# Kernel optimization log

Hardware: AMD Instinct MI355X
Metric: run time of the kernel (lower is better)

Reference implementation:

```python
import jax, jax.numpy as jnp
import numpy as np

DIM, H, KV, S, B = 2048, 16, 4, 2048, 2
HD = DIM // H
REP = H // KV
EPS = 1e-6

def rotate_half(x):
    x1, x2 = x[..., :HD // 2], x[..., HD // 2:]
    return jnp.concatenate([-x2, x1], axis=-1)

def setup_inputs() -> dict:
    key = jax.random.key(0)
    ks = jax.random.split(key, 6)
    x = jax.random.normal(ks[0], (B, S, DIM), dtype=jnp.float32)
    sc = 1.0 / np.sqrt(DIM)
    Wq = jax.random.normal(ks[1], (DIM, H * HD), dtype=jnp.float32) * sc
    Wk = jax.random.normal(ks[2], (DIM, KV * HD), dtype=jnp.float32) * sc
    Wv = jax.random.normal(ks[3], (DIM, KV * HD), dtype=jnp.float32) * sc
    Wo = jax.random.normal(ks[4], (H * HD, DIM), dtype=jnp.float32) * sc
    qg = jnp.ones((HD,), dtype=jnp.float32)
    kg = jnp.ones((HD,), dtype=jnp.float32)
    # RoPE tables (cached buffers in the torch module)
    inv_freq = 1.0 / (10000.0 ** (jnp.arange(0, HD, 2, dtype=jnp.float32) / HD))
    freqs = jnp.arange(S, dtype=jnp.float32)[:, None] * inv_freq[None, :]
    emb = jnp.concatenate([freqs, freqs], axis=-1)  # [S, HD]
    cos, sin = jnp.cos(emb), jnp.sin(emb)
    # causal additive mask [1,1,S,S]
    mask = jnp.where(jnp.tril(jnp.ones((S, S), dtype=bool)), 0.0, -1e9)[None, None].astype(jnp.float32)
    return {"x": x, "Wq": Wq, "Wk": Wk, "Wv": Wv, "Wo": Wo,
            "qg": qg, "kg": kg, "cos": cos, "sin": sin, "mask": mask}

def rmsnorm(x, g):
    rms = jnp.sqrt(jnp.mean(x * x, axis=-1, keepdims=True) + EPS)
    return g * (x / rms)

def reference(x, Wq, Wk, Wv, Wo, qg, kg, cos, sin, mask):
    Bx, Sx, _ = x.shape
    q = (x @ Wq).reshape(Bx, Sx, H, HD).transpose(0, 2, 1, 3)   # [B,H,S,HD]
    k = (x @ Wk).reshape(Bx, Sx, KV, HD).transpose(0, 2, 1, 3)  # [B,KV,S,HD]
    v = (x @ Wv).reshape(Bx, Sx, KV, HD).transpose(0, 2, 1, 3)
    q = rmsnorm(q, qg)
    k = rmsnorm(k, kg)
    c = cos[None, None, :Sx, :]
    s = sin[None, None, :Sx, :]
    q = q * c + rotate_half(q) * s
    k = k * c + rotate_half(k) * s
    k = jnp.repeat(k, REP, axis=1)  # [B,H,S,HD]
    v = jnp.repeat(v, REP, axis=1)
    scale = 1.0 / np.sqrt(HD)
    scores = jnp.einsum('bhqd,bhkd->bhqk', q, k) * scale + mask
    attn = jax.nn.softmax(scores, axis=-1)
    out = jnp.einsum('bhqk,bhkd->bhqd', attn, v)
    out = out.transpose(0, 2, 1, 3).reshape(Bx, Sx, H * HD)
    return out @ Wo
```

## Files before the change

### kernel.cpp

```cpp
#include <hip/hip_runtime.h>

typedef unsigned short u16;
typedef __attribute__((ext_vector_type(8))) short s16x8;
typedef __attribute__((ext_vector_type(4))) float f32x4;
typedef __attribute__((ext_vector_type(4))) unsigned short u16x4;

#define DIMSZ 2048
#define NH    16
#define NKV   4
#define SEQ   2048
#define BB    2
#define HD    128
#define REPF  4
#define SCALE 0.08838834764831845f

__device__ __forceinline__ u16 f2bf(float x) {
  union { float f; unsigned u; } v; v.f = x;
  unsigned r = v.u + 0x7fffu + ((v.u >> 16) & 1u);
  return (u16)(r >> 16);
}
__device__ __forceinline__ float bf2f(u16 x) {
  union { unsigned u; float f; } v; v.u = ((unsigned)x) << 16;
  return v.f;
}
__device__ __forceinline__ unsigned pack2(float a, float b) {
  union { float f; unsigned u; } x, y; x.f = a; y.f = b;
  return ((x.u + 0x8000u) >> 16) | ((y.u + 0x8000u) & 0xffff0000u);
}
__device__ __forceinline__ void gld16(const void* g, void* l) {
  __builtin_amdgcn_global_load_lds(
      (const __attribute__((address_space(1))) unsigned int*)g,
      (__attribute__((address_space(3))) unsigned int*)l, 16, 0, 0);
}

#define BARX __builtin_amdgcn_s_barrier()
#define LG0  do { asm volatile("s_waitcnt lgkmcnt(0)" ::: "memory"); \
                  __builtin_amdgcn_sched_barrier(0); } while (0)
#define VMW(n) asm volatile("s_waitcnt vmcnt(" #n ")" ::: "memory")

__global__ __launch_bounds__(256) void k_cvt(const float* __restrict__ x,
                                             u16* __restrict__ o) {
  int i = (blockIdx.x * 256 + threadIdx.x) * 8;
  float4 a = *(const float4*)(x + i);
  float4 b = *(const float4*)(x + i + 4);
  u16x4 p0 = { f2bf(a.x), f2bf(a.y), f2bf(a.z), f2bf(a.w) };
  u16x4 p1 = { f2bf(b.x), f2bf(b.y), f2bf(b.z), f2bf(b.w) };
  *(u16x4*)(o + i) = p0;
  *(u16x4*)(o + i + 4) = p1;
}

__global__ __launch_bounds__(256) void k_transpose(const float* __restrict__ W,
                                                   u16* __restrict__ Wt,
                                                   int K, int N) {
  __shared__ float t[32][33];
  int tx = threadIdx.x & 31, ty = threadIdx.x >> 5;
  int r0 = blockIdx.y * 32, c0 = blockIdx.x * 32;
#pragma unroll
  for (int i = 0; i < 32; i += 8)
    t[ty + i][tx] = W[(size_t)(r0 + ty + i) * N + c0 + tx];
  __syncthreads();
#pragma unroll
  for (int i = 0; i < 32; i += 8)
    Wt[(size_t)(c0 + ty + i) * K + r0 + tx] = f2bf(t[tx][ty + i]);
}

__global__ __launch_bounds__(512, 2) void k_gemm256(const u16* __restrict__ A,
                                                    const u16* __restrict__ Bt,
                                                    void* __restrict__ C0,
                                                    void* __restrict__ C1,
                                                    void* __restrict__ C2,
                                                    int M, int N, int K, int mode) {
  __shared__ __align__(16) u16 shA[2][256 * 64];
  __shared__ __align__(16) u16 shB[2][256 * 64];
  const int tid = threadIdx.x;
  const int wave = tid >> 6, lane = tid & 63;
  const int l15 = lane & 15, lh = lane >> 4;
  const int wm = wave >> 2, wn = wave & 3;
  const int m0 = blockIdx.y * 256, n0 = blockIdx.x * 256;

  const int srow = wave * 8 + (lane >> 3);
  const int sgr = ((lane & 7) ^ ((lane >> 3) & 7)) * 8;
  const u16* gA = A + (size_t)(m0 + srow) * K + sgr;
  const u16* gB = Bt + (size_t)(n0 + srow) * K + sgr;

  auto stgA = [&](int rb, int kt, int sl) {
    gld16(gA + (size_t)rb * 64 * K + (size_t)kt * 64, &shA[sl][rb * 4096 + wave * 512]);
  };
  auto stgB = [&](int rb, int kt, int sl) {
    gld16(gB + (size_t)rb * 64 * K + (size_t)kt * 64, &shB[sl][rb * 4096 + wave * 512]);
  };
  auto rdA = [&](int mf, int ks, int sl) -> s16x8 {
    int rl = wm * 128 + mf * 16 + l15;
    return *(const s16x8*)&shA[sl][rl * 64 + (((ks * 4 + lh) ^ (l15 & 7)) * 8)];
  };
  auto rdB = [&](int nf, int ks, int sl) -> s16x8 {
    int rl = wn * 64 + nf * 16 + l15;
    return *(const s16x8*)&shB[sl][rl * 64 + (((ks * 4 + lh) ^ (l15 & 7)) * 8)];
  };

  f32x4 acc[8][4] = {};
  s16x8 afr[4], bfr[4];
  const int NK = K >> 6;

  stgB(0, 0, 0); stgB(1, 0, 0); stgB(2, 0, 0); stgB(3, 0, 0);
  stgA(0, 0, 0); stgA(2, 0, 0); stgA(1, 0, 0); stgA(3, 0, 0);
  VMW(2);
  BARX;

  for (int t = 0; t < NK; ++t) {
    const int sl = t & 1, ns = sl ^ 1;
    const bool st = (t + 1 < NK);
    const int kn = t + 1;

#pragma unroll
    for (int nf = 0; nf < 4; nf++) bfr[nf] = rdB(nf, 0, sl);
#pragma unroll
    for (int i = 0; i < 4; i++) afr[i] = rdA(i, 0, sl);
    if (st) { stgB(0, kn, ns); stgB(1, kn, ns); }
    BARX; LG0;
    __builtin_amdgcn_s_setprio(1);
#pragma unroll
    for (int i = 0; i < 4; i++)
#pragma unroll
      for (int nf = 0; nf < 4; nf++)
        acc[i][nf] = __builtin_amdgcn_mfma_f32_16x16x32_bf16(afr[i], bfr[nf], acc[i][nf], 0, 0, 0);
    __builtin_amdgcn_s_setprio(0);
    if (st) VMW(2); else VMW(0);
    BARX;

#pragma unroll
    for (int i = 0; i < 4; i++) afr[i] = rdA(4 + i, 0, sl);
    if (st) { stgB(2, kn, ns); stgB(3, kn, ns); }
    BARX; LG0;
    __builtin_amdgcn_s_setprio(1);
#pragma unroll
    for (int i = 0; i < 4; i++)
#pragma unroll
      for (int nf = 0; nf < 4; nf++)
        acc[4 + i][nf] = __builtin_amdgcn_mfma_f32_16x16x32_bf16(afr[i], bfr[nf], acc[4 + i][nf], 0, 0, 0);
    __builtin_amdgcn_s_setprio(0);
    BARX;

#pragma unroll
    for (int nf = 0; nf < 4; nf++) bfr[nf] = rdB(nf, 1, sl);
#pragma unroll
    for (int i = 0; i < 4; i++) afr[i] = rdA(i, 1, sl);
    if (st) { stgA(0, kn, ns); stgA(2, kn, ns); }
    BARX; LG0;
    __builtin_amdgcn_s_setprio(1);
#pragma unroll
    for (int i = 0; i < 4; i++)
#pragma unroll
      for (int nf = 0; nf < 4; nf++)
        acc[i][nf] = __builtin_amdgcn_mfma_f32_16x16x32_bf16(afr[i], bfr[nf], acc[i][nf], 0, 0, 0);
    __builtin_amdgcn_s_setprio(0);
    BARX;

#pragma unroll
    for (int i = 0; i < 4; i++) afr[i] = rdA(4 + i, 1, sl);
    if (st) { stgA(1, kn, ns); stgA(3, kn, ns); }
    BARX; LG0;
    __builtin_amdgcn_s_setprio(1);
#pragma unroll
    for (int i = 0; i < 4; i++)
#pragma unroll
      for (int nf = 0; nf < 4; nf++)
        acc[4 + i][nf] = __builtin_amdgcn_mfma_f32_16x16x32_bf16(afr[i], bfr[nf], acc[4 + i][nf], 0, 0, 0);
    __builtin_amdgcn_s_setprio(0);
    if (st) VMW(2);
    BARX;
  }

  if (mode == 1) {
    float* C = (float*)C0;
#pragma unroll
    for (int mf = 0; mf < 8; mf++)
#pragma unroll
      for (int nf = 0; nf < 4; nf++)
#pragma unroll
        for (int r = 0; r < 4; r++) {
          int m = m0 + wm * 128 + mf * 16 + lh * 4 + r;
          int n = n0 + wn * 64 + nf * 16 + l15;
          C[(size_t)m * N + n] = acc[mf][nf][r];
        }
  } else {
    if (n0 < 2048) {
      u16* C = (u16*)C0;
#pragma unroll
      for (int mf = 0; mf < 8; mf++)
#pragma unroll
        for (int nf = 0; nf < 4; nf++)
#pragma unroll
          for (int r = 0; r < 4; r++) {
            int m = m0 + wm * 128 + mf * 16 + lh * 4 + r;
            int n = n0 + wn * 64 + nf * 16 + l15;
            C[(size_t)m * 2048 + n] = f2bf(acc[mf][nf][r]);
          }
    } else if (n0 < 2560) {
      u16* C = (u16*)C1;
#pragma unroll
      for (int mf = 0; mf < 8; mf++)
#pragma unroll
        for (int nf = 0; nf < 4; nf++)
#pragma unroll
          for (int r = 0; r < 4; r++) {
            int m = m0 + wm * 128 + mf * 16 + lh * 4 + r;
            int n = n0 - 2048 + wn * 64 + nf * 16 + l15;
            C[(size_t)m * 512 + n] = f2bf(acc[mf][nf][r]);
          }
    } else {
      u16* C = (u16*)C2;
#pragma unroll
      for (int mf = 0; mf < 8; mf++)
#pragma unroll
        for (int nf = 0; nf < 4; nf++) {
          int n = n0 - 2560 + wn * 64 + nf * 16 + l15;
          int kvh = n >> 7, d = n & 127;
          int m = m0 + wm * 128 + mf * 16 + lh * 4;
          int b = m >> 11, s = m & 2047;
          u16x4 pk = { f2bf(acc[mf][nf][0]), f2bf(acc[mf][nf][1]),
                       f2bf(acc[mf][nf][2]), f2bf(acc[mf][nf][3]) };
          *(u16x4*)&C[(((size_t)b * NKV + kvh) * HD + d) * SEQ + s] = pk;
        }
    }
  }
}

__global__ __launch_bounds__(256) void k_normrope(u16* __restrict__ Q,
                                                  u16* __restrict__ Kb,
                                                  const float* __restrict__ qg,
                                                  const float* __restrict__ kg,
                                                  const float* __restrict__ cosT,
                                                  const float* __restrict__ sinT) {
  int wid = (blockIdx.x * 256 + threadIdx.x) >> 6;
  int lane = threadIdx.x & 63;
  const int NQR = BB * SEQ * NH;
  u16* ptr; const float* g; int s;
  if (wid < NQR) {
    ptr = Q + (size_t)wid * HD; g = qg; s = (wid / NH) % SEQ;
  } else {
    int r2 = wid - NQR;
    ptr = Kb + (size_t)r2 * HD; g = kg; s = (r2 / NKV) % SEQ;
  }
  int d = lane * 2;
  unsigned v = *(const unsigned*)(ptr + d);
  float x0 = bf2f((u16)(v & 0xffff)), x1 = bf2f((u16)(v >> 16));
  float ss = x0 * x0 + x1 * x1;
#pragma unroll
  for (int off = 32; off >= 1; off >>= 1) ss += __shfl_xor(ss, off);
  float rinv = rsqrtf(ss * (1.0f / HD) + 1e-6f);
  float2 gv = *(const float2*)&g[d];
  float n0 = x0 * rinv * gv.x, n1 = x1 * rinv * gv.y;
  float p0 = __shfl_xor(n0, 32), p1 = __shfl_xor(n1, 32);
  float r0 = (lane < 32) ? -p0 : p0;
  float r1 = (lane < 32) ? -p1 : p1;
  float2 cc = *(const float2*)&cosT[s * HD + d];
  float2 sn = *(const float2*)&sinT[s * HD + d];
  float o0 = n0 * cc.x + r0 * sn.x, o1 = n1 * cc.y + r1 * sn.y;
  *(unsigned*)(ptr + d) = (unsigned)f2bf(o0) | ((unsigned)f2bf(o1) << 16);
}

__global__ __launch_bounds__(512, 2) void k_attn(const u16* __restrict__ Q,
                                                 const u16* __restrict__ Kb,
                                                 const u16* __restrict__ Vt,
                                                 u16* __restrict__ O) {
  __shared__ __align__(16) u16 shK[2][64 * 128];
  __shared__ __align__(16) u16 shV[2][128 * 64];
  __shared__ __align__(16) u16 shP[8][16 * 72];
  const int tid = threadIdx.x, wave = tid >> 6, lane = tid & 63;
  const int l15 = lane & 15, lh = lane >> 4;
  const int bid = blockIdx.x;
  const int qt = 15 - (bid >> 5);
  const int bh = bid & 31, b = bh >> 4, h = bh & 15, kvh = h >> 2;
  const int q0w = qt * 128 + wave * 16;

  const u16* qbase = Q + ((size_t)((size_t)b * SEQ + q0w + l15) * NH + h) * HD;
  s16x8 qf[4];
#pragma unroll
  for (int kf = 0; kf < 4; kf++) qf[kf] = *(const s16x8*)(qbase + kf * 32 + lh * 8);

  const u16* srcK[2]; const u16* srcV[2];
  int dstK[2], dstV[2];
#pragma unroll
  for (int c = 0; c < 2; c++) {
    int rk = c * 32 + wave * 4 + (lane >> 4);
    int gk = (lane & 15) ^ (rk & 7);
    srcK[c] = Kb + ((size_t)((size_t)b * SEQ + rk) * NKV + kvh) * HD + gk * 8;
    dstK[c] = (c * 32 + wave * 4) * 128;
    int rv = c * 64 + wave * 8 + (lane >> 3);
    int gv = (lane & 7) ^ (rv & 7);
    srcV[c] = Vt + ((size_t)((size_t)b * NKV + kvh) * HD + rv) * SEQ + gv * 8;
    dstV[c] = (c * 64 + wave * 8) * 64;
  }

  f32x4 oacc[8] = {};
  float m = -3e38f, l = 0.f;
  const int nt = qt * 2 + 2;
  const int tmask = q0w >> 6;
  const float SC2 = SCALE * 1.44269504f;

#pragma unroll
  for (int c = 0; c < 2; c++) {
    gld16(srcK[c], &shK[0][dstK[c]]);
    gld16(srcV[c], &shV[0][dstV[c]]);
  }
  __syncthreads();

  int buf = 0;
  for (int kt = 0; kt < nt; kt++) {
    if (kt + 1 < nt) {
      const size_t koff = (size_t)(kt + 1) * 64;
#pragma unroll
      for (int c = 0; c < 2; c++) {
        gld16(srcK[c] + koff * (NKV * HD), &shK[buf ^ 1][dstK[c]]);
        gld16(srcV[c] + koff, &shV[buf ^ 1][dstV[c]]);
      }
    }

    f32x4 sacc[4] = {};
    __builtin_amdgcn_s_setprio(1);
#pragma unroll
    for (int kf = 0; kf < 4; kf++)
#pragma unroll
      for (int nf = 0; nf < 4; nf++) {
        s16x8 kfr = *(const s16x8*)&shK[buf][(nf * 16 + l15) * 128 + (((kf * 4 + lh) ^ (l15 & 7)) * 8)];
        sacc[nf] = __builtin_amdgcn_mfma_f32_16x16x32_bf16(kfr, qf[kf], sacc[nf], 0, 0, 0);
      }
    __builtin_amdgcn_s_setprio(0);

    const int q = q0w + l15;
    float p[4][4];
    float mx = -3e38f;
    if (kt >= tmask) {
#pragma unroll
      for (int nf = 0; nf < 4; nf++)
#pragma unroll
        for (int r = 0; r < 4; r++) {
          int k = kt * 64 + nf * 16 + lh * 4 + r;
          float s = (k <= q) ? sacc[nf][r] * SC2 : -3e38f;
          p[nf][r] = s; mx = fmaxf(mx, s);
        }
    } else {
#pragma unroll
      for (int nf = 0; nf < 4; nf++)
#pragma unroll
        for (int r = 0; r < 4; r++) {
          float s = sacc[nf][r] * SC2;
          p[nf][r] = s; mx = fmaxf(mx, s);
        }
    }
    mx = fmaxf(mx, __shfl_xor(mx, 16));
    mx = fmaxf(mx, __shfl_xor(mx, 32));

    if (!__all(mx - m <= 8.0f)) {
      float mnew = fmaxf(m, mx);
      float alpha = exp2f(m - mnew);
      l *= alpha; m = mnew;
#pragma unroll
      for (int r = 0; r < 4; r++) {
        float ar = __shfl(alpha, (lh << 2) | r);
#pragma unroll
        for (int nf = 0; nf < 8; nf++) oacc[nf][r] *= ar;
      }
    }

    float rs = 0.f;
#pragma unroll
    for (int nf = 0; nf < 4; nf++)
#pragma unroll
      for (int r = 0; r < 4; r++) {
        float pe = exp2f(p[nf][r] - m);
        p[nf][r] = pe; rs += pe;
      }
    rs += __shfl_xor(rs, 16);
    rs += __shfl_xor(rs, 32);
    l += rs;

    u16* pw = &shP[wave][l15 * 72];
#pragma unroll
    for (int nf = 0; nf < 4; nf++) {
      uint2 w2 = { pack2(p[nf][0], p[nf][1]), pack2(p[nf][2], p[nf][3]) };
      *(uint2*)(pw + nf * 16 + lh * 4) = w2;
    }
    LG0;

    __builtin_amdgcn_s_setprio(1);
#pragma unroll
    for (int kvf = 0; kvf < 2; kvf++) {
      s16x8 pf = *(const s16x8*)&shP[wave][l15 * 72 + kvf * 32 + lh * 8];
#pragma unroll
      for (int nf = 0; nf < 8; nf++) {
        s16x8 vf = *(const s16x8*)&shV[buf][(nf * 16 + l15) * 64 + (((kvf * 4 + lh) ^ (l15 & 7)) * 8)];
        oacc[nf] = __builtin_amdgcn_mfma_f32_16x16x32_bf16(pf, vf, oacc[nf], 0, 0, 0);
      }
    }
    __builtin_amdgcn_s_setprio(0);
    __syncthreads();
    buf ^= 1;
  }

#pragma unroll
  for (int r = 0; r < 4; r++) {
    float lv = __shfl(l, (lh << 2) | r);
    float linv = 1.0f / lv;
    int s = q0w + lh * 4 + r;
    u16* orow = O + ((size_t)((size_t)b * SEQ + s) * NH + h) * HD;
#pragma unroll
    for (int nf = 0; nf < 8; nf++)
      orow[nf * 16 + l15] = f2bf(oacc[nf][r] * linv);
  }
}

extern "C" void kernel_launch(void* const* d_in, const int* in_sizes, int n_in,
                              void* d_out, int out_size, void* d_ws, size_t ws_size,
                              hipStream_t stream) {
  const float* x    = (const float*)d_in[0];
  const float* Wq   = (const float*)d_in[1];
  const float* Wk   = (const float*)d_in[2];
  const float* Wv   = (const float*)d_in[3];
  const float* Wo   = (const float*)d_in[4];
  const float* qg   = (const float*)d_in[5];
  const float* kg   = (const float*)d_in[6];
  const float* cosT = (const float*)d_in[7];
  const float* sinT = (const float*)d_in[8];

  char* ws = (char*)d_ws;
  const size_t MB = 1024 * 1024;
  u16* xb    = (u16*)(ws);
  u16* Wqkvt = (u16*)(ws + 16 * MB);
  u16* Wot   = (u16*)(ws + 28 * MB);
  u16* Qb    = (u16*)(ws + 36 * MB);
  u16* Kbf   = (u16*)(ws + 52 * MB);
  u16* Vt    = (u16*)(ws + 56 * MB);
  u16* Ob    = xb;

  k_cvt<<<4096, 256, 0, stream>>>(x, xb);
  k_transpose<<<dim3(DIMSZ / 32, DIMSZ / 32), 256, 0, stream>>>(Wq, Wqkvt, DIMSZ, DIMSZ);
  k_transpose<<<dim3(512 / 32, DIMSZ / 32), 256, 0, stream>>>(Wk, Wqkvt + (size_t)2048 * 2048, DIMSZ, 512);
  k_transpose<<<dim3(512 / 32, DIMSZ / 32), 256, 0, stream>>>(Wv, Wqkvt + (size_t)2560 * 2048, DIMSZ, 512);
  k_transpose<<<dim3(DIMSZ / 32, DIMSZ / 32), 256, 0, stream>>>(Wo, Wot, DIMSZ, DIMSZ);

  k_gemm256<<<dim3(12, 16), 512, 0, stream>>>(xb, Wqkvt, Qb, Kbf, Vt,
                                              BB * SEQ, 3072, DIMSZ, 3);

  k_normrope<<<20480, 256, 0, stream>>>(Qb, Kbf, qg, kg, cosT, sinT);
  k_attn<<<512, 512, 0, stream>>>(Qb, Kbf, Vt, Ob);

  k_gemm256<<<dim3(8, 16), 512, 0, stream>>>(Ob, Wot, (float*)d_out, nullptr, nullptr,
                                             BB * SEQ, DIMSZ, DIMSZ, 1);
}
```

Before: 367.5 us.

## Retile GEMM to 256x128 triple-buffered and rewrite attention with 32x32 MFMA

The GEMM tile shrinks from 256x256 to 256x128 with a three-stage LDS pipeline that prefetches two k-tiles ahead, doubling the grid to fill more CUs. The attention kernel moves to 256-thread blocks where each wave handles 32 queries using 32x32x16 MFMAs. It keeps P in registers via v_cvt_pk_bf16_f32 and v_permlane32_swap instead of round-tripping through shared memory, and skips fully masked key tiles. The changes risk higher register pressure, and less data reuse per GEMM tile.

```diff
diff --git a/kernel.cpp b/kernel.cpp
--- a/kernel.cpp
+++ b/kernel.cpp
@@ -3,7 +3,9 @@
 typedef unsigned short u16;
 typedef __attribute__((ext_vector_type(8))) short s16x8;
 typedef __attribute__((ext_vector_type(4))) float f32x4;
+typedef __attribute__((ext_vector_type(16))) float f32x16;
 typedef __attribute__((ext_vector_type(4))) unsigned short u16x4;
+typedef __attribute__((ext_vector_type(4))) unsigned int ui32x4;
 
 #define DIMSZ 2048
 #define NH    16
@@ -23,10 +25,6 @@
   union { unsigned u; float f; } v; v.u = ((unsigned)x) << 16;
   return v.f;
 }
-__device__ __forceinline__ unsigned pack2(float a, float b) {
-  union { float f; unsigned u; } x, y; x.f = a; y.f = b;
-  return ((x.u + 0x8000u) >> 16) | ((y.u + 0x8000u) & 0xffff0000u);
-}
 __device__ __forceinline__ void gld16(const void* g, void* l) {
   __builtin_amdgcn_global_load_lds(
       (const __attribute__((address_space(1))) unsigned int*)g,
@@ -36,7 +34,10 @@
 #define BARX __builtin_amdgcn_s_barrier()
 #define LG0  do { asm volatile("s_waitcnt lgkmcnt(0)" ::: "memory"); \
                   __builtin_amdgcn_sched_barrier(0); } while (0)
-#define VMW(n) asm volatile("s_waitcnt vmcnt(" #n ")" ::: "memory")
+#define VMW(n) do { asm volatile("s_waitcnt vmcnt(" #n ")" ::: "memory"); \
+                    __builtin_amdgcn_sched_barrier(0); } while (0)
+#define CVTPK(d, a, b) asm("v_cvt_pk_bf16_f32 %0, %1, %2" : "=v"(d) : "v"(a), "v"(b))
+#define SWAP32(a, b)   asm("v_permlane32_swap_b32 %0, %1" : "+v"(a), "+v"(b))
 
 __global__ __launch_bounds__(256) void k_cvt(const float* __restrict__ x,
                                              u16* __restrict__ o) {
@@ -64,122 +65,100 @@
     Wt[(size_t)(c0 + ty + i) * K + r0 + tx] = f2bf(t[tx][ty + i]);
 }
 
-__global__ __launch_bounds__(512, 2) void k_gemm256(const u16* __restrict__ A,
-                                                    const u16* __restrict__ Bt,
-                                                    void* __restrict__ C0,
-                                                    void* __restrict__ C1,
-                                                    void* __restrict__ C2,
-                                                    int M, int N, int K, int mode) {
-  __shared__ __align__(16) u16 shA[2][256 * 64];
-  __shared__ __align__(16) u16 shB[2][256 * 64];
+__global__ __launch_bounds__(512, 2) void k_gemm(const u16* __restrict__ A,
+                                                 const u16* __restrict__ Bt,
+                                                 void* __restrict__ C0,
+                                                 void* __restrict__ C1,
+                                                 void* __restrict__ C2,
+                                                 int M, int N, int K, int mode) {
+  __shared__ __align__(16) u16 shA[3][256 * 64];
+  __shared__ __align__(16) u16 shB[3][128 * 64];
   const int tid = threadIdx.x;
   const int wave = tid >> 6, lane = tid & 63;
   const int l15 = lane & 15, lh = lane >> 4;
-  const int wm = wave >> 2, wn = wave & 3;
-  const int m0 = blockIdx.y * 256, n0 = blockIdx.x * 256;
+  const int wm = wave >> 1, wn = wave & 1;
+  const int m0 = blockIdx.y * 256, n0 = blockIdx.x * 128;
 
   const int srow = wave * 8 + (lane >> 3);
-  const int sgr = ((lane & 7) ^ ((lane >> 3) & 7)) * 8;
+  const int sgr = ((lane & 7) ^ (srow & 7)) * 8;
   const u16* gA = A + (size_t)(m0 + srow) * K + sgr;
   const u16* gB = Bt + (size_t)(n0 + srow) * K + sgr;
 
-  auto stgA = [&](int rb, int kt, int sl) {
-    gld16(gA + (size_t)rb * 64 * K + (size_t)kt * 64, &shA[sl][rb * 4096 + wave * 512]);
+  auto stgA = [&](int u, int kt, int sl) {
+    gld16(gA + (size_t)u * 64 * K + (size_t)kt * 64, &shA[sl][u * 4096 + wave * 512]);
   };
-  auto stgB = [&](int rb, int kt, int sl) {
-    gld16(gB + (size_t)rb * 64 * K + (size_t)kt * 64, &shB[sl][rb * 4096 + wave * 512]);
+  auto stgB = [&](int u, int kt, int sl) {
+    gld16(gB + (size_t)u * 64 * K + (size_t)kt * 64, &shB[sl][u * 4096 + wave * 512]);
   };
   auto rdA = [&](int mf, int ks, int sl) -> s16x8 {
-    int rl = wm * 128 + mf * 16 + l15;
-    return *(const s16x8*)&shA[sl][rl * 64 + (((ks * 4 + lh) ^ (l15 & 7)) * 8)];
+    int r = wm * 64 + mf * 16 + l15;
+    return *(const s16x8*)&shA[sl][r * 64 + (((ks * 4 + lh) ^ (r & 7)) * 8)];
   };
   auto rdB = [&](int nf, int ks, int sl) -> s16x8 {
-    int rl = wn * 64 + nf * 16 + l15;
-    return *(const s16x8*)&shB[sl][rl * 64 + (((ks * 4 + lh) ^ (l15 & 7)) * 8)];
+    int r = wn * 64 + nf * 16 + l15;
+    return *(const s16x8*)&shB[sl][r * 64 + (((ks * 4 + lh) ^ (r & 7)) * 8)];
   };
 
-  f32x4 acc[8][4] = {};
-  s16x8 afr[4], bfr[4];
+  f32x4 acc[4][4] = {};
   const int NK = K >> 6;
 
-  stgB(0, 0, 0); stgB(1, 0, 0); stgB(2, 0, 0); stgB(3, 0, 0);
-  stgA(0, 0, 0); stgA(2, 0, 0); stgA(1, 0, 0); stgA(3, 0, 0);
-  VMW(2);
+#pragma unroll
+  for (int u = 0; u < 4; u++) stgA(u, 0, 0);
+  stgB(0, 0, 0); stgB(1, 0, 0);
+#pragma unroll
+  for (int u = 0; u < 4; u++) stgA(u, 1, 1);
+  stgB(0, 1, 1); stgB(1, 1, 1);
+  VMW(6);
   BARX;
 
+  int sl = 0, s1 = 1, s2 = 2;
   for (int t = 0; t < NK; ++t) {
-    const int sl = t & 1, ns = sl ^ 1;
-    const bool st = (t + 1 < NK);
-    const int kn = t + 1;
-
-#pragma unroll
-    for (int nf = 0; nf < 4; nf++) bfr[nf] = rdB(nf, 0, sl);
-#pragma unroll
-    for (int i = 0; i < 4; i++) afr[i] = rdA(i, 0, sl);
-    if (st) { stgB(0, kn, ns); stgB(1, kn, ns); }
+    const bool st2 = (t + 2 < NK);
+    s16x8 af[4], bf[4];
+
+#pragma unroll
+    for (int i = 0; i < 4; i++) af[i] = rdA(i, 0, sl);
+#pragma unroll
+    for (int i = 0; i < 4; i++) bf[i] = rdB(i, 0, sl);
+    if (st2) { stgA(0, t + 2, s2); stgA(1, t + 2, s2); stgA(2, t + 2, s2); }
     BARX; LG0;
     __builtin_amdgcn_s_setprio(1);
 #pragma unroll
     for (int i = 0; i < 4; i++)
 #pragma unroll
-      for (int nf = 0; nf < 4; nf++)
-        acc[i][nf] = __builtin_amdgcn_mfma_f32_16x16x32_bf16(afr[i], bfr[nf], acc[i][nf], 0, 0, 0);
+      for (int j = 0; j < 4; j++)
+        acc[i][j] = __builtin_amdgcn_mfma_f32_16x16x32_bf16(af[i], bf[j], acc[i][j], 0, 0, 0);
     __builtin_amdgcn_s_setprio(0);
-    if (st) VMW(2); else VMW(0);
     BARX;
 
 #pragma unroll
-    for (int i = 0; i < 4; i++) afr[i] = rdA(4 + i, 0, sl);
-    if (st) { stgB(2, kn, ns); stgB(3, kn, ns); }
+    for (int i = 0; i < 4; i++) af[i] = rdA(i, 1, sl);
+#pragma unroll
+    for (int i = 0; i < 4; i++) bf[i] = rdB(i, 1, sl);
+    if (st2) { stgA(3, t + 2, s2); stgB(0, t + 2, s2); stgB(1, t + 2, s2); }
     BARX; LG0;
     __builtin_amdgcn_s_setprio(1);
 #pragma unroll
     for (int i = 0; i < 4; i++)
 #pragma unroll
-      for (int nf = 0; nf < 4; nf++)
-        acc[4 + i][nf] = __builtin_amdgcn_mfma_f32_16x16x32_bf16(afr[i], bfr[nf], acc[4 + i][nf], 0, 0, 0);
+      for (int j = 0; j < 4; j++)
+        acc[i][j] = __builtin_amdgcn_mfma_f32_16x16x32_bf16(af[i], bf[j], acc[i][j], 0, 0, 0);
     __builtin_amdgcn_s_setprio(0);
+    if (t + 2 < NK)      { VMW(6); }
+    else if (t + 1 < NK) { VMW(0); }
     BARX;
-
-#pragma unroll
-    for (int nf = 0; nf < 4; nf++) bfr[nf] = rdB(nf, 1, sl);
-#pragma unroll
-    for (int i = 0; i < 4; i++) afr[i] = rdA(i, 1, sl);
-    if (st) { stgA(0, kn, ns); stgA(2, kn, ns); }
-    BARX; LG0;
-    __builtin_amdgcn_s_setprio(1);
-#pragma unroll
-    for (int i = 0; i < 4; i++)
-#pragma unroll
-      for (int nf = 0; nf < 4; nf++)
-        acc[i][nf] = __builtin_amdgcn_mfma_f32_16x16x32_bf16(afr[i], bfr[nf], acc[i][nf], 0, 0, 0);
-    __builtin_amdgcn_s_setprio(0);
-    BARX;
-
-#pragma unroll
-    for (int i = 0; i < 4; i++) afr[i] = rdA(4 + i, 1, sl);
-    if (st) { stgA(1, kn, ns); stgA(3, kn, ns); }
-    BARX; LG0;
-    __builtin_amdgcn_s_setprio(1);
-#pragma unroll
-    for (int i = 0; i < 4; i++)
-#pragma unroll
-      for (int nf = 0; nf < 4; nf++)
-        acc[4 + i][nf] = __builtin_amdgcn_mfma_f32_16x16x32_bf16(afr[i], bfr[nf], acc[4 + i][nf], 0, 0, 0);
-    __builtin_amdgcn_s_setprio(0);
-    if (st) VMW(2);
-    BARX;
+    int tmp = sl; sl = s1; s1 = s2; s2 = tmp;
   }
 
   if (mode == 1) {
     float* C = (float*)C0;
 #pragma unroll
-    for (int mf = 0; mf < 8; mf++)
+    for (int mf = 0; mf < 4; mf++)
 #pragma unroll
       for (int nf = 0; nf < 4; nf++)
 #pragma unroll
         for (int r = 0; r < 4; r++) {
-          int m = m0 + wm * 128 + mf * 16 + lh * 4 + r;
+          int m = m0 + wm * 64 + mf * 16 + lh * 4 + r;
           int n = n0 + wn * 64 + nf * 16 + l15;
           C[(size_t)m * N + n] = acc[mf][nf][r];
         }
@@ -187,36 +166,36 @@
     if (n0 < 2048) {
       u16* C = (u16*)C0;
 #pragma unroll
-      for (int mf = 0; mf < 8; mf++)
+      for (int mf = 0; mf < 4; mf++)
 #pragma unroll
         for (int nf = 0; nf < 4; nf++)
 #pragma unroll
           for (int r = 0; r < 4; r++) {
-            int m = m0 + wm * 128 + mf * 16 + lh * 4 + r;
+            int m = m0 + wm * 64 + mf * 16 + lh * 4 + r;
             int n = n0 + wn * 64 + nf * 16 + l15;
             C[(size_t)m * 2048 + n] = f2bf(acc[mf][nf][r]);
           }
     } else if (n0 < 2560) {
       u16* C = (u16*)C1;
 #pragma unroll
-      for (int mf = 0; mf < 8; mf++)
+      for (int mf = 0; mf < 4; mf++)
 #pragma unroll
         for (int nf = 0; nf < 4; nf++)
 #pragma unroll
           for (int r = 0; r < 4; r++) {
-            int m = m0 + wm * 128 + mf * 16 + lh * 4 + r;
+            int m = m0 + wm * 64 + mf * 16 + lh * 4 + r;
             int n = n0 - 2048 + wn * 64 + nf * 16 + l15;
             C[(size_t)m * 512 + n] = f2bf(acc[mf][nf][r]);
           }
     } else {
       u16* C = (u16*)C2;
 #pragma unroll
-      for (int mf = 0; mf < 8; mf++)
+      for (int mf = 0; mf < 4; mf++)
 #pragma unroll
         for (int nf = 0; nf < 4; nf++) {
           int n = n0 - 2560 + wn * 64 + nf * 16 + l15;
           int kvh = n >> 7, d = n & 127;
-          int m = m0 + wm * 128 + mf * 16 + lh * 4;
+          int m = m0 + wm * 64 + mf * 16 + lh * 4;
           int b = m >> 11, s = m & 2047;
           u16x4 pk = { f2bf(acc[mf][nf][0]), f2bf(acc[mf][nf][1]),
                        f2bf(acc[mf][nf][2]), f2bf(acc[mf][nf][3]) };
@@ -260,155 +239,160 @@
   *(unsigned*)(ptr + d) = (unsigned)f2bf(o0) | ((unsigned)f2bf(o1) << 16);
 }
 
-__global__ __launch_bounds__(512, 2) void k_attn(const u16* __restrict__ Q,
+__global__ __launch_bounds__(256, 2) void k_attn(const u16* __restrict__ Q,
                                                  const u16* __restrict__ Kb,
                                                  const u16* __restrict__ Vt,
                                                  u16* __restrict__ O) {
   __shared__ __align__(16) u16 shK[2][64 * 128];
   __shared__ __align__(16) u16 shV[2][128 * 64];
-  __shared__ __align__(16) u16 shP[8][16 * 72];
   const int tid = threadIdx.x, wave = tid >> 6, lane = tid & 63;
-  const int l15 = lane & 15, lh = lane >> 4;
+  const int l31 = lane & 31, hi = lane >> 5;
   const int bid = blockIdx.x;
   const int qt = 15 - (bid >> 5);
   const int bh = bid & 31, b = bh >> 4, h = bh & 15, kvh = h >> 2;
-  const int q0w = qt * 128 + wave * 16;
-
-  const u16* qbase = Q + ((size_t)((size_t)b * SEQ + q0w + l15) * NH + h) * HD;
-  s16x8 qf[4];
-#pragma unroll
-  for (int kf = 0; kf < 4; kf++) qf[kf] = *(const s16x8*)(qbase + kf * 32 + lh * 8);
-
-  const u16* srcK[2]; const u16* srcV[2];
-  int dstK[2], dstV[2];
-#pragma unroll
-  for (int c = 0; c < 2; c++) {
-    int rk = c * 32 + wave * 4 + (lane >> 4);
+  const int q0w = qt * 128 + wave * 32;
+  const int q = q0w + l31;
+
+  const u16* qbase = Q + ((size_t)((size_t)b * SEQ + q) * NH + h) * HD + hi * 8;
+  s16x8 qf[8];
+#pragma unroll
+  for (int s = 0; s < 8; s++) qf[s] = *(const s16x8*)(qbase + s * 16);
+
+  const u16* srcK[4]; const u16* srcV[4]; int dstK[4], dstV[4];
+#pragma unroll
+  for (int u = 0; u < 4; u++) {
+    int rk = u * 16 + wave * 4 + (lane >> 4);
     int gk = (lane & 15) ^ (rk & 7);
-    srcK[c] = Kb + ((size_t)((size_t)b * SEQ + rk) * NKV + kvh) * HD + gk * 8;
-    dstK[c] = (c * 32 + wave * 4) * 128;
-    int rv = c * 64 + wave * 8 + (lane >> 3);
+    srcK[u] = Kb + ((size_t)((size_t)b * SEQ + rk) * NKV + kvh) * HD + gk * 8;
+    dstK[u] = (u * 16 + wave * 4) * 128;
+    int rv = u * 32 + wave * 8 + (lane >> 3);
     int gv = (lane & 7) ^ (rv & 7);
-    srcV[c] = Vt + ((size_t)((size_t)b * NKV + kvh) * HD + rv) * SEQ + gv * 8;
-    dstV[c] = (c * 64 + wave * 8) * 64;
+    srcV[u] = Vt + ((size_t)((size_t)b * NKV + kvh) * HD + rv) * SEQ + gv * 8;
+    dstV[u] = (u * 32 + wave * 8) * 64;
   }
 
-  f32x4 oacc[8] = {};
+  f32x16 oacc[4] = {};
   float m = -3e38f, l = 0.f;
   const int nt = qt * 2 + 2;
   const int tmask = q0w >> 6;
+  const int tlast = (q0w + 31) >> 6;
   const float SC2 = SCALE * 1.44269504f;
 
 #pragma unroll
-  for (int c = 0; c < 2; c++) {
-    gld16(srcK[c], &shK[0][dstK[c]]);
-    gld16(srcV[c], &shV[0][dstV[c]]);
-  }
+  for (int u = 0; u < 4; u++) { gld16(srcK[u], &shK[0][dstK[u]]); gld16(srcV[u], &shV[0][dstV[u]]); }
   __syncthreads();
 
   int buf = 0;
   for (int kt = 0; kt < nt; kt++) {
     if (kt + 1 < nt) {
-      const size_t koff = (size_t)(kt + 1) * 64;
-#pragma unroll
-      for (int c = 0; c < 2; c++) {
-        gld16(srcK[c] + koff * (NKV * HD), &shK[buf ^ 1][dstK[c]]);
-        gld16(srcV[c] + koff, &shV[buf ^ 1][dstV[c]]);
+      const size_t ko = (size_t)(kt + 1) * 64;
+#pragma unroll
+      for (int u = 0; u < 4; u++) {
+        gld16(srcK[u] + ko * (NKV * HD), &shK[buf ^ 1][dstK[u]]);
+        gld16(srcV[u] + ko, &shV[buf ^ 1][dstV[u]]);
       }
     }
 
-    f32x4 sacc[4] = {};
-    __builtin_amdgcn_s_setprio(1);
-#pragma unroll
-    for (int kf = 0; kf < 4; kf++)
-#pragma unroll
-      for (int nf = 0; nf < 4; nf++) {
-        s16x8 kfr = *(const s16x8*)&shK[buf][(nf * 16 + l15) * 128 + (((kf * 4 + lh) ^ (l15 & 7)) * 8)];
-        sacc[nf] = __builtin_amdgcn_mfma_f32_16x16x32_bf16(kfr, qf[kf], sacc[nf], 0, 0, 0);
+    if (kt <= tlast) {
+      f32x16 sacc[2] = {};
+      __builtin_amdgcn_s_setprio(1);
+#pragma unroll
+      for (int s = 0; s < 8; s++)
+#pragma unroll
+        for (int tt = 0; tt < 2; tt++) {
+          int r = tt * 32 + l31;
+          s16x8 kf = *(const s16x8*)&shK[buf][r * 128 + (((s * 2 + hi) ^ (r & 7)) * 8)];
+          sacc[tt] = __builtin_amdgcn_mfma_f32_32x32x16_bf16(kf, qf[s], sacc[tt], 0, 0, 0);
+        }
+      __builtin_amdgcn_s_setprio(0);
+
+      float pv[2][16];
+      float mx = -3e38f;
+      const int kbase = kt * 64 + 4 * hi;
+      if (kt >= tmask) {
+#pragma unroll
+        for (int tt = 0; tt < 2; tt++)
+#pragma unroll
+          for (int r = 0; r < 16; r++) {
+            int kvv = kbase + tt * 32 + (r & 3) + 8 * (r >> 2);
+            float v = (kvv <= q) ? sacc[tt][r] * SC2 : -3e38f;
+            pv[tt][r] = v; mx = fmaxf(mx, v);
+          }
+      } else {
+#pragma unroll
+        for (int tt = 0; tt < 2; tt++)
+#pragma unroll
+          for (int r = 0; r < 16; r++) {
+            float v = sacc[tt][r] * SC2;
+            pv[tt][r] = v; mx = fmaxf(mx, v);
+          }
       }
-    __builtin_amdgcn_s_setprio(0);
-
-    const int q = q0w + l15;
-    float p[4][4];
-    float mx = -3e38f;
-    if (kt >= tmask) {
-#pragma unroll
-      for (int nf = 0; nf < 4; nf++)
-#pragma unroll
-        for (int r = 0; r < 4; r++) {
-          int k = kt * 64 + nf * 16 + lh * 4 + r;
-          float s = (k <= q) ? sacc[nf][r] * SC2 : -3e38f;
-          p[nf][r] = s; mx = fmaxf(mx, s);
-        }
-    } else {
-#pragma unroll
-      for (int nf = 0; nf < 4; nf++)
-#pragma unroll
-        for (int r = 0; r < 4; r++) {
-          float s = sacc[nf][r] * SC2;
-          p[nf][r] = s; mx = fmaxf(mx, s);
-        }
+      mx = fmaxf(mx, __shfl_xor(mx, 32));
+
+      if (!__all(mx - m <= 8.0f)) {
+        float mnew = fmaxf(m, mx);
+        float al = exp2f(m - mnew);
+        l *= al; m = mnew;
+#pragma unroll
+        for (int dt = 0; dt < 4; dt++)
+#pragma unroll
+          for (int r = 0; r < 16; r++) oacc[dt][r] *= al;
+      }
+
+      float rs = 0.f;
+#pragma unroll
+      for (int tt = 0; tt < 2; tt++)
+#pragma unroll
+        for (int r = 0; r < 16; r++) {
+          float pe = exp2f(pv[tt][r] - m);
+          pv[tt][r] = pe; rs += pe;
+        }
+      rs += __shfl_xor(rs, 32);
+      l += rs;
+
+      s16x8 pa[4];
+#pragma unroll
+      for (int tt = 0; tt < 2; tt++)
+#pragma unroll
+        for (int hf = 0; hf < 2; hf++) {
+          unsigned w0, w1, w2, w3;
+          CVTPK(w0, pv[tt][hf * 8 + 0], pv[tt][hf * 8 + 1]);
+          CVTPK(w1, pv[tt][hf * 8 + 2], pv[tt][hf * 8 + 3]);
+          CVTPK(w2, pv[tt][hf * 8 + 4], pv[tt][hf * 8 + 5]);
+          CVTPK(w3, pv[tt][hf * 8 + 6], pv[tt][hf * 8 + 7]);
+          SWAP32(w0, w2);
+          SWAP32(w1, w3);
+          ui32x4 t4 = { w0, w1, w2, w3 };
+          pa[tt * 2 + hf] = *(s16x8*)&t4;
+        }
+
+      __builtin_amdgcn_s_setprio(1);
+#pragma unroll
+      for (int sp = 0; sp < 4; sp++)
+#pragma unroll
+        for (int dt = 0; dt < 4; dt++) {
+          int r = dt * 32 + l31;
+          s16x8 vf = *(const s16x8*)&shV[buf][r * 64 + (((sp * 2 + hi) ^ (r & 7)) * 8)];
+          oacc[dt] = __builtin_amdgcn_mfma_f32_32x32x16_bf16(vf, pa[sp], oacc[dt], 0, 0, 0);
+        }
+      __builtin_amdgcn_s_setprio(0);
     }
-    mx = fmaxf(mx, __shfl_xor(mx, 16));
-    mx = fmaxf(mx, __shfl_xor(mx, 32));
-
-    if (!__all(mx - m <= 8.0f)) {
-      float mnew = fmaxf(m, mx);
-      float alpha = exp2f(m - mnew);
-      l *= alpha; m = mnew;
-#pragma unroll
-      for (int r = 0; r < 4; r++) {
-        float ar = __shfl(alpha, (lh << 2) | r);
-#pragma unroll
-        for (int nf = 0; nf < 8; nf++) oacc[nf][r] *= ar;
-      }
-    }
-
-    float rs = 0.f;
-#pragma unroll
-    for (int nf = 0; nf < 4; nf++)
-#pragma unroll
-      for (int r = 0; r < 4; r++) {
-        float pe = exp2f(p[nf][r] - m);
-        p[nf][r] = pe; rs += pe;
-      }
-    rs += __shfl_xor(rs, 16);
-    rs += __shfl_xor(rs, 32);
-    l += rs;
-
-    u16* pw = &shP[wave][l15 * 72];
-#pragma unroll
-    for (int nf = 0; nf < 4; nf++) {
-      uint2 w2 = { pack2(p[nf][0], p[nf][1]), pack2(p[nf][2], p[nf][3]) };
-      *(uint2*)(pw + nf * 16 + lh * 4) = w2;
-    }
-    LG0;
-
-    __builtin_amdgcn_s_setprio(1);
-#pragma unroll
-    for (int kvf = 0; kvf < 2; kvf++) {
-      s16x8 pf = *(const s16x8*)&shP[wave][l15 * 72 + kvf * 32 + lh * 8];
-#pragma unroll
-      for (int nf = 0; nf < 8; nf++) {
-        s16x8 vf = *(const s16x8*)&shV[buf][(nf * 16 + l15) * 64 + (((kvf * 4 + lh) ^ (l15 & 7)) * 8)];
-        oacc[nf] = __builtin_amdgcn_mfma_f32_16x16x32_bf16(pf, vf, oacc[nf], 0, 0, 0);
-      }
-    }
-    __builtin_amdgcn_s_setprio(0);
+
     __syncthreads();
     buf ^= 1;
   }
 
-#pragma unroll
-  for (int r = 0; r < 4; r++) {
-    float lv = __shfl(l, (lh << 2) | r);
-    float linv = 1.0f / lv;
-    int s = q0w + lh * 4 + r;
-    u16* orow = O + ((size_t)((size_t)b * SEQ + s) * NH + h) * HD;
-#pragma unroll
-    for (int nf = 0; nf < 8; nf++)
-      orow[nf * 16 + l15] = f2bf(oacc[nf][r] * linv);
-  }
+  float linv = 1.0f / l;
+  u16* orow = O + ((size_t)((size_t)b * SEQ + q) * NH + h) * HD;
+#pragma unroll
+  for (int dt = 0; dt < 4; dt++)
+#pragma unroll
+    for (int rg = 0; rg < 4; rg++) {
+      int d = dt * 32 + 8 * rg + 4 * hi;
+      u16x4 pk4 = { f2bf(oacc[dt][rg * 4 + 0] * linv), f2bf(oacc[dt][rg * 4 + 1] * linv),
+                    f2bf(oacc[dt][rg * 4 + 2] * linv), f2bf(oacc[dt][rg * 4 + 3] * linv) };
+      *(u16x4*)(orow + d) = pk4;
+    }
 }
 
 extern "C" void kernel_launch(void* const* d_in, const int* in_sizes, int n_in,
@@ -440,12 +424,12 @@
   k_transpose<<<dim3(512 / 32, DIMSZ / 32), 256, 0, stream>>>(Wv, Wqkvt + (size_t)2560 * 2048, DIMSZ, 512);
   k_transpose<<<dim3(DIMSZ / 32, DIMSZ / 32), 256, 0, stream>>>(Wo, Wot, DIMSZ, DIMSZ);
 
-  k_gemm256<<<dim3(12, 16), 512, 0, stream>>>(xb, Wqkvt, Qb, Kbf, Vt,
-                                              BB * SEQ, 3072, DIMSZ, 3);
+  k_gemm<<<dim3(24, 16), 512, 0, stream>>>(xb, Wqkvt, Qb, Kbf, Vt,
+                                           BB * SEQ, 3072, DIMSZ, 3);
 
   k_normrope<<<20480, 256, 0, stream>>>(Qb, Kbf, qg, kg, cosT, sinT);
-  k_attn<<<512, 512, 0, stream>>>(Qb, Kbf, Vt, Ob);
-
-  k_gemm256<<<dim3(8, 16), 512, 0, stream>>>(Ob, Wot, (float*)d_out, nullptr, nullptr,
-                                             BB * SEQ, DIMSZ, DIMSZ, 1);
-}
+  k_attn<<<512, 256, 0, stream>>>(Qb, Kbf, Vt, Ob);
+
+  k_gemm<<<dim3(16, 16), 512, 0, stream>>>(Ob, Wot, (float*)d_out, nullptr, nullptr,
+                                           BB * SEQ, DIMSZ, DIMSZ, 1);
+}
```

Result: faster. 349.1 us (-5.0%).
